# Optimization experiments

Measured on AMD Instinct MI355X. Metric: run time of the kernel, lower is better.

The kernel has to match this reference:

```python
import jax, jax.numpy as jnp
import numpy as np

N_NODES = 50000
N_EDGES = 800000
DIM = 128
N_LAYERS = 4
EPS = 1e-5  # BatchNorm1d default eps


def setup_inputs() -> dict:
    key = jax.random.key(0)
    k_x, k_e, k_w = jax.random.split(key, 3)
    x = jax.random.normal(k_x, (N_NODES, DIM), dtype=jnp.float32)
    edge_index = jax.random.randint(k_e, (2, N_EDGES), 0, N_NODES, dtype=jnp.int32)
    # stacked per-layer params (input_dim == hidden_dim == DIM)
    Ws = jax.random.normal(k_w, (N_LAYERS, DIM, DIM), dtype=jnp.float32) * (1.0 / np.sqrt(DIM))
    bs = jnp.zeros((N_LAYERS, DIM), jnp.float32)
    gammas = jnp.ones((N_LAYERS, DIM), jnp.float32)
    betas = jnp.zeros((N_LAYERS, DIM), jnp.float32)
    return {"x": x, "edge_index": edge_index, "Ws": Ws, "bs": bs,
            "gammas": gammas, "betas": betas}


def gcn_conv(x, W, b, src, dst, n):
    # PyG GCNConv: h = X W; out = D^{-1/2}(A+I)D^{-1/2} h + b
    h = x @ W                                       # [N, D]
    deg = jnp.zeros((n,), h.dtype).at[dst].add(1.0) + 1.0  # +1 self-loop
    dis = jax.lax.rsqrt(deg)                        # deg > 0 due to self-loops
    msg = h[src] * (dis[src] * dis[dst])[:, None]   # [E, D] gather + scale
    out = jnp.zeros_like(h).at[dst].add(msg)        # scatter-add aggregate
    out = out + h * (dis * dis)[:, None]            # self-loop term, norm = 1/deg
    return out + b


def batchnorm(z, gamma, beta):
    # BatchNorm1d training-mode math: batch mean, biased variance
    mu = z.mean(axis=0)
    var = z.var(axis=0)
    return (z - mu) * jax.lax.rsqrt(var + EPS) * gamma + beta


def reference(x, edge_index, Ws, bs, gammas, betas):
    src, dst = edge_index[0], edge_index[1]
    z = x
    for i in range(N_LAYERS):
        z = gcn_conv(z, Ws[i], bs[i], src, dst, z.shape[0])
        z = jax.nn.relu(z)
        z = batchnorm(z, gammas[i], betas[i])
        # Dropout: identity (eval mode / deterministic reference)
    return z
```

## Files before the change

### kernel.cpp

```cpp
#include <hip/hip_runtime.h>

#define N_NODES 50000
#define N_EDGES 800000
#define DIM 128
#define NLAYERS 4
#define BN_EPS 1e-5f
#define SCAN_BLOCKS 196

__device__ __forceinline__ float bf2f(unsigned short u){
    union { unsigned int i; float f; } x; x.i = ((unsigned int)u) << 16; return x.f;
}
__device__ __forceinline__ unsigned short f2bf(float f){
    union { float f; unsigned int i; } x; x.f = f;
    unsigned int lsb = (x.i >> 16) & 1u;
    unsigned int r = x.i + 0x7fffu + lsb;
    return (unsigned short)(r >> 16);
}


__global__ __launch_bounds__(256) void k_zero(int* __restrict__ p, int n){
    int i = blockIdx.x * 256 + threadIdx.x;
    if (i < n) p[i] = 0;
}

__global__ __launch_bounds__(256) void k_count(const int* __restrict__ dst,
                                               int* __restrict__ degcnt){
    int e = blockIdx.x * 256 + threadIdx.x;
    if (e < N_EDGES) atomicAdd(&degcnt[dst[e]], 1);
}

__global__ __launch_bounds__(256) void k_dis(const int* __restrict__ degcnt,
                                             float* __restrict__ dis){
    int i = blockIdx.x * 256 + threadIdx.x;
    if (i < N_NODES) dis[i] = rsqrtf((float)degcnt[i] + 1.0f);
}

__global__ __launch_bounds__(256) void k_scan1(const int* __restrict__ degcnt,
                                               int* __restrict__ rowptr,
                                               int* __restrict__ bsum){
    __shared__ int tmp[256];
    int t = threadIdx.x;
    int i = blockIdx.x * 256 + t;
    int v = (i < N_NODES) ? degcnt[i] : 0;
    tmp[t] = v;
    __syncthreads();
    #pragma unroll
    for (int off = 1; off < 256; off <<= 1){
        int u = (t >= off) ? tmp[t - off] : 0;
        __syncthreads();
        tmp[t] += u;
        __syncthreads();
    }
    if (i < N_NODES) rowptr[i] = tmp[t] - v;
    if (t == 255) bsum[blockIdx.x] = tmp[255];
}

__global__ __launch_bounds__(256) void k_scan2(int* __restrict__ bsum){
    __shared__ int tmp[256];
    int t = threadIdx.x;
    int v = (t < SCAN_BLOCKS) ? bsum[t] : 0;
    tmp[t] = v;
    __syncthreads();
    #pragma unroll
    for (int off = 1; off < 256; off <<= 1){
        int u = (t >= off) ? tmp[t - off] : 0;
        __syncthreads();
        tmp[t] += u;
        __syncthreads();
    }
    if (t < SCAN_BLOCKS) bsum[t] = tmp[t] - v;
}

__global__ __launch_bounds__(256) void k_scan3(const int* __restrict__ bsum,
                                               int* __restrict__ rowptr,
                                               int* __restrict__ wptr){
    int i = blockIdx.x * 256 + threadIdx.x;
    if (i < N_NODES){
        int r = rowptr[i] + bsum[blockIdx.x];
        rowptr[i] = r; wptr[i] = r;
    }
    if (i == 0) rowptr[N_NODES] = N_EDGES;
}

__global__ __launch_bounds__(256) void k_fill(const int* __restrict__ src,
                                              const int* __restrict__ dst,
                                              const float* __restrict__ dis,
                                              int* __restrict__ wptr,
                                              int2* __restrict__ epair){
    int e = blockIdx.x * 256 + threadIdx.x;
    if (e < N_EDGES){
        int s = src[e], d = dst[e];
        float w = dis[s] * dis[d];
        int p = atomicAdd(&wptr[d], 1);
        int2 pr; pr.x = s; pr.y = __float_as_int(w);
        epair[p] = pr;
    }
}


template<int MODE>
__global__ __launch_bounds__(256) void k_gemm(const void* __restrict__ zraw,
                                              const float* __restrict__ W,
                                              const float* __restrict__ scsh,
                                              unsigned short* __restrict__ hb){
    __shared__ float zs[32][DIM];
    int tid = threadIdx.x;
    int row0 = blockIdx.x * 32;

    if (MODE == 0){
        const float4* zv = (const float4*)zraw;
        float4* zsv = (float4*)(&zs[0][0]);
        #pragma unroll
        for (int i = 0; i < 4; i++){
            int idx = tid + 256*i;
            int r = idx >> 5;
            float4 val = make_float4(0.f, 0.f, 0.f, 0.f);
            if (row0 + r < N_NODES) val = zv[row0*32 + idx];
            zsv[idx] = val;
        }
    } else {
        const uint4* zv = (const uint4*)zraw;
        #pragma unroll
        for (int i = 0; i < 2; i++){
            int idx = tid + 256*i;
            int r = idx >> 4;
            int c = (idx & 15) * 8;
            int gg = c >> 5, wi = c & 31;
            uint4 raw = make_uint4(0,0,0,0);
            int row = row0 + r;
            if (row < N_NODES) raw = zv[gg*(N_NODES*4) + row*4 + (wi >> 3)];
            float4 sc0 = *(const float4*)&scsh[c];
            float4 sc1 = *(const float4*)&scsh[c + 4];
            float4 sh0 = *(const float4*)&scsh[DIM + c];
            float4 sh1 = *(const float4*)&scsh[DIM + c + 4];
            unsigned int u[4] = {raw.x, raw.y, raw.z, raw.w};
            float v[8];
            #pragma unroll
            for (int j = 0; j < 4; j++){
                v[2*j]   = bf2f((unsigned short)(u[j] & 0xffff));
                v[2*j+1] = bf2f((unsigned short)(u[j] >> 16));
            }
            zs[r][c+0] = fmaf(v[0], sc0.x, sh0.x);
            zs[r][c+1] = fmaf(v[1], sc0.y, sh0.y);
            zs[r][c+2] = fmaf(v[2], sc0.z, sh0.z);
            zs[r][c+3] = fmaf(v[3], sc0.w, sh0.w);
            zs[r][c+4] = fmaf(v[4], sc1.x, sh1.x);
            zs[r][c+5] = fmaf(v[5], sc1.y, sh1.y);
            zs[r][c+6] = fmaf(v[6], sc1.z, sh1.z);
            zs[r][c+7] = fmaf(v[7], sc1.w, sh1.w);
        }
    }
    __syncthreads();

    int r0 = (tid >> 5) * 4;
    int c0 = (tid & 31) * 4;
    float acc[4][4] = {};

    for (int k = 0; k < DIM; k += 4){
        float4 a[4];
        #pragma unroll
        for (int r = 0; r < 4; r++) a[r] = *(const float4*)&zs[r0 + r][k];
        float4 wv[4];
        #pragma unroll
        for (int kk = 0; kk < 4; kk++)
            wv[kk] = *(const float4*)&W[(k + kk)*DIM + c0];
        #pragma unroll
        for (int r = 0; r < 4; r++){
            float av[4] = {a[r].x, a[r].y, a[r].z, a[r].w};
            #pragma unroll
            for (int kk = 0; kk < 4; kk++){
                acc[r][0] = fmaf(av[kk], wv[kk].x, acc[r][0]);
                acc[r][1] = fmaf(av[kk], wv[kk].y, acc[r][1]);
                acc[r][2] = fmaf(av[kk], wv[kk].z, acc[r][2]);
                acc[r][3] = fmaf(av[kk], wv[kk].w, acc[r][3]);
            }
        }
    }
    int gg = c0 >> 5, wi = c0 & 31;
    #pragma unroll
    for (int r = 0; r < 4; r++){
        int row = row0 + r0 + r;
        if (row < N_NODES){
            ushort4 o;
            o.x = f2bf(acc[r][0]); o.y = f2bf(acc[r][1]);
            o.z = f2bf(acc[r][2]); o.w = f2bf(acc[r][3]);
            *(ushort4*)&hb[(size_t)gg*N_NODES*32 + (size_t)row*32 + wi] = o;
        }
    }
}

__global__ __launch_bounds__(256) void k_agg(const unsigned short* __restrict__ h,
                                             const int* __restrict__ rowptr,
                                             const int2* __restrict__ epair,
                                             const float* __restrict__ dis,
                                             const float* __restrict__ bias,
                                             unsigned short* __restrict__ out,
                                             float* __restrict__ stats){
    int lane = threadIdx.x & 63;
    int w    = threadIdx.x >> 6;
    int g    = blockIdx.x & 3;
    int sub  = lane >> 4;
    int cp   = lane & 15;
    const ushort2* hg = (const ushort2*)(h + (size_t)g * N_NODES * 32);
    ushort2* og = (ushort2*)(out + (size_t)g * N_NODES * 32);
    float b0 = bias[g*32 + 2*cp], b1 = bias[g*32 + 2*cp + 1];
    float s0 = 0.f, s1 = 0.f, q0 = 0.f, q1 = 0.f;
    int bg = blockIdx.x >> 2;
    int nstride = (gridDim.x >> 2) * 4;

    for (int node = bg*4 + w; node < N_NODES; node += nstride){
        float di = dis[node];
        int e0 = rowptr[node], e1 = rowptr[node + 1];
        float pa0 = 0.f, pa1 = 0.f, pb0 = 0.f, pb1 = 0.f;
        if (sub == 0){
            ushort2 hv = hg[node*16 + cp];
            float dii = di * di;
            pa0 = bf2f(hv.x) * dii; pa1 = bf2f(hv.y) * dii;
        }
        int e = e0;
        for (; e + 8 <= e1; e += 8){
            int2 pra = epair[e + sub];
            int2 prb = epair[e + 4 + sub];
            ushort2 xa = hg[pra.x*16 + cp];
            ushort2 xb = hg[prb.x*16 + cp];
            float wa = __int_as_float(pra.y);
            float wb = __int_as_float(prb.y);
            pa0 = fmaf(bf2f(xa.x), wa, pa0);
            pa1 = fmaf(bf2f(xa.y), wa, pa1);
            pb0 = fmaf(bf2f(xb.x), wb, pb0);
            pb1 = fmaf(bf2f(xb.y), wb, pb1);
        }
        for (; e < e1; e += 4){
            int ide = e + sub;
            int2 pr = (ide < e1) ? epair[ide] : make_int2(0, 0);
            ushort2 xv = hg[pr.x*16 + cp];
            float we = __int_as_float(pr.y);
            pa0 = fmaf(bf2f(xv.x), we, pa0);
            pa1 = fmaf(bf2f(xv.y), we, pa1);
        }
        float r0 = pa0 + pb0, r1 = pa1 + pb1;
        r0 += __shfl_xor(r0, 16); r1 += __shfl_xor(r1, 16);
        r0 += __shfl_xor(r0, 32); r1 += __shfl_xor(r1, 32);
        if (sub == 0){
            float a0 = fmaxf(r0 + b0, 0.f);
            float a1 = fmaxf(r1 + b1, 0.f);
            ushort2 ov; ov.x = f2bf(a0); ov.y = f2bf(a1);
            og[node*16 + cp] = ov;
            s0 += a0; s1 += a1; q0 += a0*a0; q1 += a1*a1;
        }
    }

    __shared__ float red[4][16][4];
    if (sub == 0){
        red[w][cp][0] = s0; red[w][cp][1] = s1;
        red[w][cp][2] = q0; red[w][cp][3] = q1;
    }
    __syncthreads();
    if (w == 0 && sub == 0){
        #pragma unroll
        for (int ww = 1; ww < 4; ww++){
            s0 += red[ww][cp][0]; s1 += red[ww][cp][1];
            q0 += red[ww][cp][2]; q1 += red[ww][cp][3];
        }
        int c = g*32 + 2*cp;
        atomicAdd(&stats[c],         s0);
        atomicAdd(&stats[c + 1],     s1);
        atomicAdd(&stats[DIM + c],     q0);
        atomicAdd(&stats[DIM + c + 1], q1);
    }
}

__global__ void k_bnstat(const float* __restrict__ stats,
                         const float* __restrict__ gamma,
                         const float* __restrict__ beta,
                         float* __restrict__ scsh){
    int c = threadIdx.x;
    float mu  = stats[c] * (1.0f / N_NODES);
    float var = stats[DIM + c] * (1.0f / N_NODES) - mu * mu;
    float sc  = rsqrtf(var + BN_EPS) * gamma[c];
    scsh[c] = sc;
    scsh[DIM + c] = beta[c] - mu * sc;
}

__global__ __launch_bounds__(256) void k_bn(const uint4* __restrict__ in,
                                            const float* __restrict__ scsh,
                                            float4* __restrict__ outf){
    int i = blockIdx.x * 256 + threadIdx.x;
    if (i >= N_NODES * DIM / 8) return;
    int row = i >> 4;
    int c = (i * 8) & (DIM - 1);
    int gg = c >> 5, wi = c & 31;
    uint4 raw = in[gg*(N_NODES*4) + row*4 + (wi >> 3)];
    float4 sc0 = *(const float4*)&scsh[c];
    float4 sc1 = *(const float4*)&scsh[c + 4];
    float4 sh0 = *(const float4*)&scsh[DIM + c];
    float4 sh1 = *(const float4*)&scsh[DIM + c + 4];
    unsigned int u[4] = {raw.x, raw.y, raw.z, raw.w};
    float v[8];
    #pragma unroll
    for (int j = 0; j < 4; j++){
        v[2*j]   = bf2f((unsigned short)(u[j] & 0xffff));
        v[2*j+1] = bf2f((unsigned short)(u[j] >> 16));
    }
    float4 r0, r1;
    r0.x = fmaf(v[0], sc0.x, sh0.x);
    r0.y = fmaf(v[1], sc0.y, sh0.y);
    r0.z = fmaf(v[2], sc0.z, sh0.z);
    r0.w = fmaf(v[3], sc0.w, sh0.w);
    r1.x = fmaf(v[4], sc1.x, sh1.x);
    r1.y = fmaf(v[5], sc1.y, sh1.y);
    r1.z = fmaf(v[6], sc1.z, sh1.z);
    r1.w = fmaf(v[7], sc1.w, sh1.w);
    outf[2*i]   = r0;
    outf[2*i+1] = r1;
}


extern "C" void kernel_launch(void* const* d_in, const int* in_sizes, int n_in,
                              void* d_out, int out_size, void* d_ws, size_t ws_size,
                              hipStream_t stream){
    const float* x   = (const float*)d_in[0];
    const int*   src = (const int*)d_in[1];
    const int*   dst = src + N_EDGES;
    const float* Ws  = (const float*)d_in[2];
    const float* bs  = (const float*)d_in[3];
    const float* gs  = (const float*)d_in[4];
    const float* be  = (const float*)d_in[5];

    char* w = (char*)d_ws;
    int*   degcnt = (int*)(w);
    float* stats  = (float*)(w + 200000);
    float* scsh   = (float*)(w + 204096);
    float* dis    = (float*)(w + 208192);
    int*   rowptr = (int*)(w + 408192);
    int*   wptr   = (int*)(w + 608208);
    int*   bsum   = (int*)(w + 808208);
    int2*  epair  = (int2*)(w + 809232);
    unsigned short* bufA = (unsigned short*)(w + 7209232);
    unsigned short* hb   = (unsigned short*)(w + 20009232);

    k_zero<<<(51024 + 255)/256, 256, 0, stream>>>(degcnt, 51024);
    k_count<<<3125, 256, 0, stream>>>(dst, degcnt);
    k_dis<<<196, 256, 0, stream>>>(degcnt, dis);
    k_scan1<<<SCAN_BLOCKS, 256, 0, stream>>>(degcnt, rowptr, bsum);
    k_scan2<<<1, 256, 0, stream>>>(bsum);
    k_scan3<<<SCAN_BLOCKS, 256, 0, stream>>>(bsum, rowptr, wptr);
    k_fill<<<3125, 256, 0, stream>>>(src, dst, dis, wptr, epair);

    for (int L = 0; L < NLAYERS; L++){
        if (L == 0)
            k_gemm<0><<<1563, 256, 0, stream>>>(x, Ws + L*DIM*DIM,
                                                nullptr, hb);
        else
            k_gemm<1><<<1563, 256, 0, stream>>>(bufA, Ws + L*DIM*DIM,
                                                scsh + (L-1)*256, hb);
        k_agg<<<2048, 256, 0, stream>>>(hb, rowptr, epair, dis, bs + L*DIM,
                                        bufA, stats + L*256);
        k_bnstat<<<1, 128, 0, stream>>>(stats + L*256, gs + L*DIM, be + L*DIM,
                                        scsh + L*256);
    }
    k_bn<<<3125, 256, 0, stream>>>((const uint4*)bufA, scsh + 3*256,
                                   (float4*)d_out);
}
```

Baseline: 658.5 us.

## Use bf16 MFMA GEMM with split-W precision and folded BatchNorm affine

Replaces the FP32 FMA GEMM with a bf16 MFMA 16x16x32 kernel. W is split into hi and lo bf16 parts to keep precision, and the previous layer's BN scale is folded into W and its shift into a precomputed bias vector. The input x is converted once to a grouped bf16 layout, and the aggregation inner loop is unrolled to 16 edges with four accumulators to expose more memory parallelism. This adds small per-layer prep kernels and a conversion pass. Activations now enter the GEMM as bf16, and x itself is rounded to bf16.

```diff
diff --git a/kernel.cpp b/kernel.cpp
--- a/kernel.cpp
+++ b/kernel.cpp
@@ -6,6 +6,10 @@
 #define NLAYERS 4
 #define BN_EPS 1e-5f
 #define SCAN_BLOCKS 196
+#define WSTRIDE 136
+
+typedef __attribute__((ext_vector_type(8))) short short8;
+typedef __attribute__((ext_vector_type(4))) float f32x4;
 
 __device__ __forceinline__ float bf2f(unsigned short u){
     union { unsigned int i; float f; } x; x.i = ((unsigned int)u) << 16; return x.f;
@@ -97,94 +101,114 @@
     }
 }
 
-
-template<int MODE>
-__global__ __launch_bounds__(256) void k_gemm(const void* __restrict__ zraw,
-                                              const float* __restrict__ W,
-                                              const float* __restrict__ scsh,
+__global__ __launch_bounds__(256) void k_cvt(const float* __restrict__ x,
+                                             unsigned short* __restrict__ xg){
+    int i = blockIdx.x * 256 + threadIdx.x;
+    if (i >= N_NODES * 16) return;
+    int row = i >> 4;
+    int c = (i & 15) * 8;
+    float4 v0 = *(const float4*)&x[row*DIM + c];
+    float4 v1 = *(const float4*)&x[row*DIM + c + 4];
+    int g = c >> 5, wi = c & 31;
+    ushort4 o0, o1;
+    o0.x = f2bf(v0.x); o0.y = f2bf(v0.y); o0.z = f2bf(v0.z); o0.w = f2bf(v0.w);
+    o1.x = f2bf(v1.x); o1.y = f2bf(v1.y); o1.z = f2bf(v1.z); o1.w = f2bf(v1.w);
+    unsigned short* p = &xg[(size_t)g*N_NODES*32 + (size_t)row*32 + wi];
+    *(ushort4*)p = o0;
+    *(ushort4*)(p + 4) = o1;
+}
+
+template<bool HAS>
+__global__ __launch_bounds__(256) void k_wprep(const float* __restrict__ W,
+                                               const float* __restrict__ scsh,
+                                               unsigned short* __restrict__ wthi,
+                                               unsigned short* __restrict__ wtlo){
+    int idx = blockIdx.x * 256 + threadIdx.x;
+    int c = idx >> 7, k = idx & 127;
+    float v = W[k*DIM + c];
+    if (HAS) v *= scsh[k];
+    unsigned short hi = f2bf(v);
+    float lo = v - bf2f(hi);
+    wthi[c*DIM + k] = hi;
+    wtlo[c*DIM + k] = f2bf(lo);
+}
+
+template<bool HAS>
+__global__ __launch_bounds__(128) void k_wbias(const float* __restrict__ W,
+                                               const float* __restrict__ scsh,
+                                               float* __restrict__ bias2){
+    int c = threadIdx.x;
+    float acc = 0.f;
+    if (HAS){
+        #pragma unroll 4
+        for (int k = 0; k < DIM; k++)
+            acc = fmaf(scsh[DIM + k], W[k*DIM + c], acc);
+    }
+    bias2[c] = acc;
+}
+
+
+__global__ __launch_bounds__(256) void k_gemm(const unsigned short* __restrict__ zg,
+                                              const unsigned short* __restrict__ wthi,
+                                              const unsigned short* __restrict__ wtlo,
+                                              const float* __restrict__ bias2,
                                               unsigned short* __restrict__ hb){
-    __shared__ float zs[32][DIM];
+    __shared__ short whi[DIM * WSTRIDE];
+    __shared__ short wlo[DIM * WSTRIDE];
     int tid = threadIdx.x;
-    int row0 = blockIdx.x * 32;
-
-    if (MODE == 0){
-        const float4* zv = (const float4*)zraw;
-        float4* zsv = (float4*)(&zs[0][0]);
+
+    {
+        const uint4* gh = (const uint4*)wthi;
+        const uint4* gl = (const uint4*)wtlo;
         #pragma unroll
-        for (int i = 0; i < 4; i++){
-            int idx = tid + 256*i;
-            int r = idx >> 5;
-            float4 val = make_float4(0.f, 0.f, 0.f, 0.f);
-            if (row0 + r < N_NODES) val = zv[row0*32 + idx];
-            zsv[idx] = val;
-        }
-    } else {
-        const uint4* zv = (const uint4*)zraw;
+        for (int it = 0; it < 8; it++){
+            int ch = tid + 256*it;
+            int c = ch >> 4, k8 = ch & 15;
+            int off = c*WSTRIDE + k8*8;
+            *(uint4*)&whi[off] = gh[ch];
+            *(uint4*)&wlo[off] = gl[ch];
+        }
+    }
+    __syncthreads();
+
+    int lane = tid & 63;
+    int wv   = tid >> 6;
+    int m = lane & 15;
+    int q = lane >> 4;
+    int row0 = blockIdx.x * 64 + wv * 16;
+    int arow = row0 + m;
+    bool avalid = arow < N_NODES;
+
+    f32x4 acc[8];
+    #pragma unroll
+    for (int t = 0; t < 8; t++) acc[t] = (f32x4){0.f, 0.f, 0.f, 0.f};
+
+    #pragma unroll
+    for (int g = 0; g < 4; g++){
+        short8 a = {0,0,0,0,0,0,0,0};
+        if (avalid)
+            a = *(const short8*)&zg[(size_t)g*N_NODES*32 + (size_t)arow*32 + q*8];
         #pragma unroll
-        for (int i = 0; i < 2; i++){
-            int idx = tid + 256*i;
-            int r = idx >> 4;
-            int c = (idx & 15) * 8;
-            int gg = c >> 5, wi = c & 31;
-            uint4 raw = make_uint4(0,0,0,0);
-            int row = row0 + r;
-            if (row < N_NODES) raw = zv[gg*(N_NODES*4) + row*4 + (wi >> 3)];
-            float4 sc0 = *(const float4*)&scsh[c];
-            float4 sc1 = *(const float4*)&scsh[c + 4];
-            float4 sh0 = *(const float4*)&scsh[DIM + c];
-            float4 sh1 = *(const float4*)&scsh[DIM + c + 4];
-            unsigned int u[4] = {raw.x, raw.y, raw.z, raw.w};
-            float v[8];
-            #pragma unroll
-            for (int j = 0; j < 4; j++){
-                v[2*j]   = bf2f((unsigned short)(u[j] & 0xffff));
-                v[2*j+1] = bf2f((unsigned short)(u[j] >> 16));
-            }
-            zs[r][c+0] = fmaf(v[0], sc0.x, sh0.x);
-            zs[r][c+1] = fmaf(v[1], sc0.y, sh0.y);
-            zs[r][c+2] = fmaf(v[2], sc0.z, sh0.z);
-            zs[r][c+3] = fmaf(v[3], sc0.w, sh0.w);
-            zs[r][c+4] = fmaf(v[4], sc1.x, sh1.x);
-            zs[r][c+5] = fmaf(v[5], sc1.y, sh1.y);
-            zs[r][c+6] = fmaf(v[6], sc1.z, sh1.z);
-            zs[r][c+7] = fmaf(v[7], sc1.w, sh1.w);
-        }
-    }
-    __syncthreads();
-
-    int r0 = (tid >> 5) * 4;
-    int c0 = (tid & 31) * 4;
-    float acc[4][4] = {};
-
-    for (int k = 0; k < DIM; k += 4){
-        float4 a[4];
-        #pragma unroll
-        for (int r = 0; r < 4; r++) a[r] = *(const float4*)&zs[r0 + r][k];
-        float4 wv[4];
-        #pragma unroll
-        for (int kk = 0; kk < 4; kk++)
-            wv[kk] = *(const float4*)&W[(k + kk)*DIM + c0];
+        for (int t = 0; t < 8; t++){
+            int col = t*16 + m;
+            int off = col*WSTRIDE + g*32 + q*8;
+            short8 bh = *(const short8*)&whi[off];
+            short8 bl = *(const short8*)&wlo[off];
+            acc[t] = __builtin_amdgcn_mfma_f32_16x16x32_bf16(a, bh, acc[t], 0, 0, 0);
+            acc[t] = __builtin_amdgcn_mfma_f32_16x16x32_bf16(a, bl, acc[t], 0, 0, 0);
+        }
+    }
+
+    #pragma unroll
+    for (int t = 0; t < 8; t++){
+        int colg = t*16 + m;
+        float bz = bias2[colg];
+        size_t base = (size_t)(t >> 1)*N_NODES*32 + (t & 1)*16 + m;
         #pragma unroll
         for (int r = 0; r < 4; r++){
-            float av[4] = {a[r].x, a[r].y, a[r].z, a[r].w};
-            #pragma unroll
-            for (int kk = 0; kk < 4; kk++){
-                acc[r][0] = fmaf(av[kk], wv[kk].x, acc[r][0]);
-                acc[r][1] = fmaf(av[kk], wv[kk].y, acc[r][1]);
-                acc[r][2] = fmaf(av[kk], wv[kk].z, acc[r][2]);
-                acc[r][3] = fmaf(av[kk], wv[kk].w, acc[r][3]);
-            }
-        }
-    }
-    int gg = c0 >> 5, wi = c0 & 31;
-    #pragma unroll
-    for (int r = 0; r < 4; r++){
-        int row = row0 + r0 + r;
-        if (row < N_NODES){
-            ushort4 o;
-            o.x = f2bf(acc[r][0]); o.y = f2bf(acc[r][1]);
-            o.z = f2bf(acc[r][2]); o.w = f2bf(acc[r][3]);
-            *(ushort4*)&hb[(size_t)gg*N_NODES*32 + (size_t)row*32 + wi] = o;
+            int row = row0 + q*4 + r;
+            if (row < N_NODES)
+                hb[base + (size_t)row*32] = f2bf(acc[t][r] + bz);
         }
     }
 }
@@ -212,23 +236,37 @@
         float di = dis[node];
         int e0 = rowptr[node], e1 = rowptr[node + 1];
         float pa0 = 0.f, pa1 = 0.f, pb0 = 0.f, pb1 = 0.f;
+        float pc0 = 0.f, pc1 = 0.f, pd0 = 0.f, pd1 = 0.f;
         if (sub == 0){
             ushort2 hv = hg[node*16 + cp];
             float dii = di * di;
             pa0 = bf2f(hv.x) * dii; pa1 = bf2f(hv.y) * dii;
         }
         int e = e0;
+        for (; e + 16 <= e1; e += 16){
+            int2 P0 = epair[e + sub];
+            int2 P1 = epair[e + 4 + sub];
+            int2 P2 = epair[e + 8 + sub];
+            int2 P3 = epair[e + 12 + sub];
+            ushort2 X0 = hg[P0.x*16 + cp];
+            ushort2 X1 = hg[P1.x*16 + cp];
+            ushort2 X2 = hg[P2.x*16 + cp];
+            ushort2 X3 = hg[P3.x*16 + cp];
+            float w0 = __int_as_float(P0.y), w1 = __int_as_float(P1.y);
+            float w2 = __int_as_float(P2.y), w3 = __int_as_float(P3.y);
+            pa0 = fmaf(bf2f(X0.x), w0, pa0); pa1 = fmaf(bf2f(X0.y), w0, pa1);
+            pb0 = fmaf(bf2f(X1.x), w1, pb0); pb1 = fmaf(bf2f(X1.y), w1, pb1);
+            pc0 = fmaf(bf2f(X2.x), w2, pc0); pc1 = fmaf(bf2f(X2.y), w2, pc1);
+            pd0 = fmaf(bf2f(X3.x), w3, pd0); pd1 = fmaf(bf2f(X3.y), w3, pd1);
+        }
         for (; e + 8 <= e1; e += 8){
-            int2 pra = epair[e + sub];
-            int2 prb = epair[e + 4 + sub];
-            ushort2 xa = hg[pra.x*16 + cp];
-            ushort2 xb = hg[prb.x*16 + cp];
-            float wa = __int_as_float(pra.y);
-            float wb = __int_as_float(prb.y);
-            pa0 = fmaf(bf2f(xa.x), wa, pa0);
-            pa1 = fmaf(bf2f(xa.y), wa, pa1);
-            pb0 = fmaf(bf2f(xb.x), wb, pb0);
-            pb1 = fmaf(bf2f(xb.y), wb, pb1);
+            int2 P0 = epair[e + sub];
+            int2 P1 = epair[e + 4 + sub];
+            ushort2 X0 = hg[P0.x*16 + cp];
+            ushort2 X1 = hg[P1.x*16 + cp];
+            float w0 = __int_as_float(P0.y), w1 = __int_as_float(P1.y);
+            pa0 = fmaf(bf2f(X0.x), w0, pa0); pa1 = fmaf(bf2f(X0.y), w0, pa1);
+            pb0 = fmaf(bf2f(X1.x), w1, pb0); pb1 = fmaf(bf2f(X1.y), w1, pb1);
         }
         for (; e < e1; e += 4){
             int ide = e + sub;
@@ -238,7 +276,8 @@
             pa0 = fmaf(bf2f(xv.x), we, pa0);
             pa1 = fmaf(bf2f(xv.y), we, pa1);
         }
-        float r0 = pa0 + pb0, r1 = pa1 + pb1;
+        float r0 = (pa0 + pb0) + (pc0 + pd0);
+        float r1 = (pa1 + pb1) + (pc1 + pd1);
         r0 += __shfl_xor(r0, 16); r1 += __shfl_xor(r1, 16);
         r0 += __shfl_xor(r0, 32); r1 += __shfl_xor(r1, 32);
         if (sub == 0){
@@ -335,9 +374,13 @@
     int*   rowptr = (int*)(w + 408192);
     int*   wptr   = (int*)(w + 608208);
     int*   bsum   = (int*)(w + 808208);
-    int2*  epair  = (int2*)(w + 809232);
-    unsigned short* bufA = (unsigned short*)(w + 7209232);
-    unsigned short* hb   = (unsigned short*)(w + 20009232);
+    float* bias2  = (float*)(w + 809232);
+    unsigned short* wthi = (unsigned short*)(w + 809744);
+    unsigned short* wtlo = (unsigned short*)(w + 842512);
+    int2*  epair  = (int2*)(w + 875280);
+    unsigned short* xg   = (unsigned short*)(w + 7275280);
+    unsigned short* bufA = (unsigned short*)(w + 20075280);
+    unsigned short* hb   = (unsigned short*)(w + 32875280);
 
     k_zero<<<(51024 + 255)/256, 256, 0, stream>>>(degcnt, 51024);
     k_count<<<3125, 256, 0, stream>>>(dst, degcnt);
@@ -346,14 +389,19 @@
     k_scan2<<<1, 256, 0, stream>>>(bsum);
     k_scan3<<<SCAN_BLOCKS, 256, 0, stream>>>(bsum, rowptr, wptr);
     k_fill<<<3125, 256, 0, stream>>>(src, dst, dis, wptr, epair);
+    k_cvt<<<3125, 256, 0, stream>>>(x, xg);
 
     for (int L = 0; L < NLAYERS; L++){
-        if (L == 0)
-            k_gemm<0><<<1563, 256, 0, stream>>>(x, Ws + L*DIM*DIM,
-                                                nullptr, hb);
-        else
-            k_gemm<1><<<1563, 256, 0, stream>>>(bufA, Ws + L*DIM*DIM,
-                                                scsh + (L-1)*256, hb);
+        const float* Wl = Ws + L*DIM*DIM;
+        if (L == 0){
+            k_wprep<false><<<64, 256, 0, stream>>>(Wl, nullptr, wthi, wtlo);
+            k_wbias<false><<<1, 128, 0, stream>>>(Wl, nullptr, bias2);
+        } else {
+            k_wprep<true><<<64, 256, 0, stream>>>(Wl, scsh + (L-1)*256, wthi, wtlo);
+            k_wbias<true><<<1, 128, 0, stream>>>(Wl, scsh + (L-1)*256, bias2);
+        }
+        const unsigned short* zin = (L == 0) ? xg : bufA;
+        k_gemm<<<(N_NODES + 63)/64, 256, 0, stream>>>(zin, wthi, wtlo, bias2, hb);
         k_agg<<<2048, 256, 0, stream>>>(hb, rowptr, epair, dis, bs + L*DIM,
                                         bufA, stats + L*256);
         k_bnstat<<<1, 128, 0, stream>>>(stats + L*256, gs + L*DIM, be + L*DIM,
```

Measured after the change: 613.5 us. -6.8%, faster.
